# Kernel tuning notes

Hardware: AMD Instinct MI355X
Metric: run time of the kernel (lower is better)

Reference implementation:

```python
import jax, jax.numpy as jnp
import numpy as np

R, S, M, K = 512, 48, 4096, 16
RADIUS = 4.0 * 0.025
DIMS = [511, 256, 256, 256, 3]


def posenc(x, n_freqs):
    freqs = 2.0 ** jnp.arange(n_freqs, dtype=x.dtype)
    xf = x[..., None, :] * freqs[:, None]            # [..., F, C]
    sc = jnp.stack([jnp.sin(xf), jnp.cos(xf)], -2)   # [..., F, 2, C]
    return jnp.concatenate([x, sc.reshape(x.shape[:-1] + (-1,))], -1)


def ball_query(q, p, radius, k):
    # pytorch3d-style: first k points (by index order) within radius.
    # dists are squared distances, 0 for padding; neighbors are 0 for padding; idx -1 for padding.
    d2 = jnp.sum((q[:, None, :] - p[None, :, :]) ** 2, -1)    # [Nq, M]
    m = p.shape[0]
    order = jnp.where(d2 < radius * radius, jnp.arange(m), m)
    neg, idx = jax.lax.top_k(-order, k)                        # k smallest valid indices
    valid = neg > -m
    dists = jnp.where(valid, jnp.take_along_axis(d2, idx, axis=1), 0.0)
    nbrs = jnp.where(valid[..., None], p[idx], 0.0)
    return dists, jnp.where(valid, idx, -1), nbrs


def setup_inputs() -> dict:
    key = jax.random.key(0)
    ks = jax.random.split(key, 16)
    inp = {
        "points": jax.random.uniform(ks[0], (R, S, 3), jnp.float32),
        "normals": jax.random.normal(ks[1], (R * S, 3), jnp.float32),
        "view_dirs": jax.random.normal(ks[2], (R * S, 3), jnp.float32),
        "feature_vectors": jax.random.normal(ks[3], (R * S, 256), jnp.float32),
        "indices": 0,
        "physical_particles": jax.random.uniform(ks[4], (M, 3), jnp.float32),
        "rays": jax.random.normal(ks[5], (R, 6), jnp.float32),
        "ro": jax.random.normal(ks[6], (1, 3), jnp.float32),
    }
    for l in range(4):
        scale = (2.0 / DIMS[l + 1]) ** 0.5
        inp[f"W{l}"] = jax.random.normal(ks[7 + l], (DIMS[l + 1], DIMS[l]), jnp.float32) * scale
        inp[f"b{l}"] = jnp.zeros((DIMS[l + 1],), jnp.float32)
    return inp


def reference(points, normals, view_dirs, feature_vectors, indices, physical_particles,
              rays, ro, W0, b0, W1, b1, W2, b2, W3, b3):
    q = points.reshape(-1, 3)                                     # [R*S, 3]
    dists, idx, nbrs = ball_query(q, physical_particles, RADIUS, K)
    dists = dists.reshape(R, S, K)
    nbrs = nbrs.reshape(R, S, K, 3)
    nn_mask = dists != 0                                          # padded entries have dist 0
    num_nn = nn_mask.sum(-1, keepdims=True)                       # [R, S, 1]

    hit_pos_emb = posenc(q, 10)                                   # [R*S, 63]
    hit_dir_emb = jnp.repeat(posenc(rays[:, 3:], 4), S, axis=0)   # [R*S, 27]

    # smoothing_position (exclude_ray=True)
    dn = jnp.linalg.norm(nbrs - points[:, :, None, :], axis=-1)   # [R, S, K]
    w = jnp.maximum(1.0 - (dn / RADIUS) ** 3, 0.0)
    density = w.sum(-1, keepdims=True)                            # [R, S, 1]
    smoothed = (w[..., None] * nbrs).sum(-2) / (density + 1e-12)  # [R, S, 3]

    sp = smoothed.reshape(-1, 3)
    dirs = sp - ro
    dirs = dirs / jnp.linalg.norm(dirs, axis=-1, keepdims=True)

    density_emb = posenc(density.reshape(-1, 1), 4)               # [R*S, 9]
    smoothed_pos_emb = posenc(sp, 10)                             # [R*S, 63]

    # masked variance of neighbor offsets
    diff = jnp.where(nn_mask[..., None], nbrs - points[:, :, None, :], 0.0)
    mean = diff.sum(-2) / (num_nn + 1e-12)
    var = jnp.where(nn_mask[..., None], (diff - mean[:, :, None, :]) ** 2, 0.0).sum(-2) / (num_nn + 1e-12)
    var_emb = posenc(var.reshape(-1, 3), 10)                      # [R*S, 63]

    x = jnp.concatenate([hit_pos_emb, density_emb, smoothed_pos_emb, var_emb,
                         hit_dir_emb, posenc(dirs, 4), normals, feature_vectors], -1)  # [R*S, 511]

    for Wl, bl in ((W0, b0), (W1, b1), (W2, b2)):
        x = jax.nn.relu(x @ Wl.T + bl)
    return jax.nn.sigmoid(x @ W3.T + b3)
```

## Files before the change

kernel.cpp:

```cpp
#include <hip/hip_runtime.h>

typedef _Float16 f16;
typedef f16 f16x8 __attribute__((ext_vector_type(8)));
typedef float f32x4 __attribute__((ext_vector_type(4)));
typedef unsigned short u16;


struct FT {
  u16 v[256];
  static constexpr u16 enc(int s, int f, int k) {
    return (u16)(s | (f << 5) | (k << 9));
  }
  constexpr void p3(int base, int F, int src) {
    v[base + 0] = enc(src + 0, 0, 0);
    v[base + 1] = enc(src + 1, 0, 0);
    v[base + 2] = enc(src + 2, 0, 0);
    for (int f = 0; f < F; ++f)
      for (int r = 0; r < 6; ++r) {
        int comp = (r < 3) ? r : r - 3;
        v[base + 3 + f * 6 + r] = enc(src + comp, f, (r < 3) ? 1 : 2);
      }
  }
  constexpr void p1(int base, int F, int src) {
    v[base] = enc(src, 0, 0);
    for (int f = 0; f < F; ++f) {
      v[base + 1 + 2 * f] = enc(src, f, 1);
      v[base + 2 + 2 * f] = enc(src, f, 2);
    }
  }
  constexpr FT() : v{} {
    p3(0, 10, 0);
    p1(63, 4, 3);
    p3(72, 10, 4);
    p3(135, 10, 7);
    p3(198, 4, 10);
    p3(225, 4, 13);
    v[252] = enc(16, 0, 0);
    v[253] = enc(17, 0, 0);
    v[254] = enc(18, 0, 0);
    v[255] = enc(0, 0, 3);
  }
};
__constant__ FT ftab = FT();

__device__ float4 g_sorted[4096];
__device__ int    g_cellStart[1001];

__global__ __launch_bounds__(1024) void setup_kernel(
    const float* __restrict__ parts,
    const float* __restrict__ W0, const float* __restrict__ W1,
    const float* __restrict__ W2,
    f16* __restrict__ w0f, f16* __restrict__ w1f, f16* __restrict__ w2f)
{
  const int tid = threadIdx.x;
  if (blockIdx.x < 256) {
    int i = blockIdx.x * 1024 + tid;
    float v; f16* pf; int n, c;
    if (i < 131072) {
      n = i >> 9; c = i & 511;
      v = (c < 255) ? W0[n * 511 + c] : ((c == 255) ? 0.0f : W0[n * 511 + (c - 1)]);
      pf = w0f;
    } else if (i < 196608) {
      int j = i - 131072; n = j >> 8; c = j & 255; v = W1[j]; pf = w1f;
    } else {
      int j = i - 196608; n = j >> 8; c = j & 255; v = W2[j]; pf = w2f;
    }
    int kt = c >> 5, g = (c >> 3) & 3, jj = c & 7;
    int u = n * 4 + (g ^ ((n >> 1) & 3));
    pf[kt * 8192 + u * 8 + jj] = (f16)v;
  } else {
    __shared__ int cnt[1000];
    __shared__ int pos[1000];
    __shared__ int wpre[125];
    for (int j = tid; j < 1000; j += 1024) cnt[j] = 0;
    __syncthreads();

    float px[4], py[4], pz[4];
    int cd[4];
    #pragma unroll
    for (int t = 0; t < 4; ++t) {
      int i = tid + t * 1024;
      float x = parts[3 * i], y = parts[3 * i + 1], z = parts[3 * i + 2];
      int cx = min(max((int)(x * 10.0f), 0), 9);
      int cy = min(max((int)(y * 10.0f), 0), 9);
      int cz = min(max((int)(z * 10.0f), 0), 9);
      cd[t] = (cz * 10 + cy) * 10 + cx;
      px[t] = x; py[t] = y; pz[t] = z;
      atomicAdd(&cnt[cd[t]], 1);
    }
    __syncthreads();

    if (tid < 125) {
      int s = 0;
      #pragma unroll
      for (int k = 0; k < 8; ++k) s += cnt[tid * 8 + k];
      wpre[tid] = s;
    }
    __syncthreads();
    if (tid == 0) {
      int s = 0;
      for (int c = 0; c < 125; ++c) { int t = wpre[c]; wpre[c] = s; s += t; }
    }
    __syncthreads();
    if (tid < 125) {
      int run = wpre[tid];
      #pragma unroll
      for (int k = 0; k < 8; ++k) {
        int c = tid * 8 + k;
        int n = cnt[c];
        pos[c] = run;
        g_cellStart[c] = run;
        run += n;
      }
    }
    if (tid == 0) g_cellStart[1000] = 4096;
    __syncthreads();

    #pragma unroll
    for (int t = 0; t < 4; ++t) {
      int p = atomicAdd(&pos[cd[t]], 1);
      g_sorted[p] = make_float4(px[t], py[t], pz[t], __int_as_float(tid + t * 1024));
    }
  }
}

#define MAXCH 5

__global__ __launch_bounds__(512, 4) void fused_all(
    const float* __restrict__ points, const float* __restrict__ normals,
    const float* __restrict__ fvec, const float* __restrict__ rays,
    const float* __restrict__ ro, const float* __restrict__ parts,
    const f16* __restrict__ w0f, const f16* __restrict__ w1f,
    const f16* __restrict__ w2f,
    const float* __restrict__ b0, const float* __restrict__ b1,
    const float* __restrict__ b2,
    const float* __restrict__ W3, const float* __restrict__ b3,
    float* __restrict__ out)
{
  extern __shared__ char lds[];
  f16* As = (f16*)lds;
  f16* Hf = (f16*)lds;
  f16* H2 = (f16*)(lds + 24576);
  float* sdata = (float*)(lds + 49152);
  float* w3s = (float*)(lds + 49152);

  const int tid = threadIdx.x, lane = tid & 63, wn = tid >> 6;
  const int l15 = lane & 15, l4 = lane >> 4;
  const int blk = blockIdx.x;

  if (tid < 384) {
    int m = tid >> 3, sub = tid & 7, g = sub & 3, kh = sub >> 2;
    int u = m * 4 + (g ^ ((m >> 1) & 3));
    #pragma unroll
    for (int t = 0; t < 4; ++t) {
      int kf = kh * 4 + t;
      const float* src = fvec + (size_t)(blk * 48 + m) * 256 + kf * 32 + g * 8;
      float4 v0 = ((const float4*)src)[0];
      float4 v1 = ((const float4*)src)[1];
      f16 hs[8] = {(f16)v0.x, (f16)v0.y, (f16)v0.z, (f16)v0.w,
                   (f16)v1.x, (f16)v1.y, (f16)v1.z, (f16)v1.w};
      *(uint4*)(As + (8 + kf) * 1536 + u * 8) = *(uint4*)hs;
    }
  }

  const float RQ = 0.1f * 0.1f;
  #pragma unroll 1
  for (int t = 0; t < 6; ++t) {
    const int m48 = wn * 6 + t;
    const int q = blk * 48 + m48;
    const float qx = points[3 * q], qy = points[3 * q + 1], qz = points[3 * q + 2];

    int nAcc = 0;
    float sdx = 0, sdy = 0, sdz = 0;
    float s2x = 0, s2y = 0, s2z = 0;
    float sw = 0, swx = 0, swy = 0, swz = 0;

    const int cqx = min(max((int)(qx * 10.0f), 0), 9);
    const int cqy = min(max((int)(qy * 10.0f), 0), 9);
    const int cqz = min(max((int)(qz * 10.0f), 0), 9);

    int st_l = 0, cn_l = 0;
    if (lane < 9) {
      int dz = lane / 3, dy = lane - dz * 3;
      int cz = cqz - 1 + dz, cy = cqy - 1 + dy;
      if ((unsigned)cz <= 9u && (unsigned)cy <= 9u) {
        int x0 = max(cqx - 1, 0), x1 = min(cqx + 1, 9);
        int rb = (cz * 10 + cy) * 10;
        st_l = g_cellStart[rb + x0];
        cn_l = g_cellStart[rb + x1 + 1] - st_l;
      }
    }

    int pk[9], bk[9];
    int run = 0;
    #pragma unroll
    for (int k = 0; k < 9; ++k) {
      int stk = __builtin_amdgcn_readlane(st_l, k);
      int cnk = __builtin_amdgcn_readlane(cn_l, k);
      pk[k] = run;
      bk[k] = stk - run;
      run += cnk;
    }
    const int C = run;
    const bool fb = (C > MAXCH * 64);

    if (!fb) {
      float4 sv[MAXCH];
      int iv[MAXCH];
      unsigned long long hm[MAXCH];
      #pragma unroll
      for (int ch = 0; ch < MAXCH; ++ch) {
        if (ch * 64 < C) {
          int s = ch * 64 + lane;
          int g = bk[0];
          #pragma unroll
          for (int k = 1; k < 9; ++k) g = (s >= pk[k]) ? bk[k] : g;
          float4 pt = g_sorted[min(g + s, 4095)];
          if (s >= C) {
            pt.x = 1e9f; pt.y = 1e9f; pt.z = 1e9f;
            pt.w = __int_as_float(0x7fffffff);
          }
          sv[ch] = pt;
          iv[ch] = __float_as_int(pt.w);
          float ex = pt.x - qx, ey = pt.y - qy, ez = pt.z - qz;
          float d2 = __fadd_rn(__fadd_rn(__fmul_rn(ex, ex), __fmul_rn(ey, ey)),
                               __fmul_rn(ez, ez));
          hm[ch] = __ballot(d2 < RQ);
        } else {
          hm[ch] = 0ULL;
        }
      }

      int N = 0;
      #pragma unroll
      for (int ch = 0; ch < MAXCH; ++ch) N += __popcll(hm[ch]);

      int thr = 0x7fffffff;
      if (N > 16) {
        int lo = 0, hi = 4095;
        while (lo < hi) {
          int mid = (lo + hi) >> 1;
          int c = 0;
          #pragma unroll
          for (int ch = 0; ch < MAXCH; ++ch)
            if (ch * 64 < C)
              c += __popcll(hm[ch] & __ballot(iv[ch] <= mid));
          if (c >= 16) hi = mid; else lo = mid + 1;
        }
        thr = lo;
      }

      #pragma unroll
      for (int ch = 0; ch < MAXCH; ++ch) {
        if (ch * 64 < C) {
          float4 pt = sv[ch];
          float ex = pt.x - qx, ey = pt.y - qy, ez = pt.z - qz;
          float d2 = __fadd_rn(__fadd_rn(__fmul_rn(ex, ex), __fmul_rn(ey, ey)),
                               __fmul_rn(ez, ez));
          if (d2 < RQ && iv[ch] <= thr) {
            nAcc++;
            sdx += ex; sdy += ey; sdz += ez;
            s2x += ex * ex; s2y += ey * ey; s2z += ez * ez;
            float dn = sqrtf(d2);
            float tt = dn * 10.0f;
            float w = fmaxf(1.0f - tt * tt * tt, 0.0f);
            sw += w; swx += w * pt.x; swy += w * pt.y; swz += w * pt.z;
          }
        }
      }
    } else {
      int total = 0;
      for (int jr = 0; jr < 64; ++jr) {
        int pi = jr * 64 + lane;
        float x = parts[3 * pi], y = parts[3 * pi + 1], z = parts[3 * pi + 2];
        float ex = x - qx, ey = y - qy, ez = z - qz;
        float d2 = __fadd_rn(__fadd_rn(__fmul_rn(ex, ex), __fmul_rn(ey, ey)),
                             __fmul_rn(ez, ez));
        bool hit = d2 < RQ;
        unsigned long long m = __ballot(hit);
        int pos = __builtin_amdgcn_mbcnt_hi((unsigned)(m >> 32),
                  __builtin_amdgcn_mbcnt_lo((unsigned)m, 0u));
        if (hit && (total + pos < 16)) {
          nAcc++;
          sdx += ex; sdy += ey; sdz += ez;
          s2x += ex * ex; s2y += ey * ey; s2z += ez * ez;
          float dn = sqrtf(d2);
          float tt = dn * 10.0f;
          float w = fmaxf(1.0f - tt * tt * tt, 0.0f);
          sw += w; swx += w * x; swy += w * y; swz += w * z;
        }
        total += __popcll(m);
        if (total >= 16) break;
      }
    }

    #define WRED(x) { _Pragma("unroll") for (int o = 32; o; o >>= 1) x += __shfl_xor(x, o, 64); }
    float fn = (float)nAcc;
    WRED(fn); WRED(sdx); WRED(sdy); WRED(sdz);
    WRED(s2x); WRED(s2y); WRED(s2z);
    WRED(sw); WRED(swx); WRED(swy); WRED(swz);
    #undef WRED

    float tq = sqrtf(qx * qx + qy * qy + qz * qz) * 10.0f;
    float wpad = fmaxf(1.0f - tq * tq * tq, 0.0f);
    float density = sw + (16.0f - fn) * wpad;
    float invd = 1.0f / (density + 1e-12f);
    float spx = swx * invd, spy = swy * invd, spz = swz * invd;

    float invn = 1.0f / (fn + 1e-12f);
    float mx = sdx * invn, my = sdy * invn, mz = sdz * invn;
    float vx = fmaxf((s2x - 2.0f * mx * sdx + fn * mx * mx) * invn, 0.0f);
    float vy = fmaxf((s2y - 2.0f * my * sdy + fn * my * my) * invn, 0.0f);
    float vz = fmaxf((s2z - 2.0f * mz * sdz + fn * mz * mz) * invn, 0.0f);

    float dxx = spx - ro[0], dyy = spy - ro[1], dzz = spz - ro[2];
    float il = 1.0f / sqrtf(dxx * dxx + dyy * dyy + dzz * dzz);

    if (lane == 0) {
      float* s = sdata + m48 * 20;
      s[0] = qx; s[1] = qy; s[2] = qz; s[3] = density;
      s[4] = spx; s[5] = spy; s[6] = spz;
      s[7] = vx; s[8] = vy; s[9] = vz;
      s[10] = rays[6 * blk + 3]; s[11] = rays[6 * blk + 4]; s[12] = rays[6 * blk + 5];
      s[13] = dxx * il; s[14] = dyy * il; s[15] = dzz * il;
      s[16] = normals[3 * q]; s[17] = normals[3 * q + 1]; s[18] = normals[3 * q + 2];
    }
  }
  __syncthreads();

  #pragma unroll 1
  for (int t = 0; t < 6; ++t) {
    const int m48 = wn * 6 + t;
    const float* s = sdata + m48 * 20;
    #pragma unroll
    for (int it = 0; it < 4; ++it) {
      int c = it * 64 + lane;
      int e = ftab.v[c];
      float sv_ = s[e & 31];
      float arg = sv_ * (float)(1 << ((e >> 5) & 15));
      float sn, cs;
      __sincosf(arg, &sn, &cs);
      int kind = e >> 9;
      float val = (kind == 0) ? sv_ : (kind == 1 ? sn : (kind == 2 ? cs : 0.0f));
      int kt = c >> 5, g = (c >> 3) & 3, j = c & 7;
      int u = m48 * 4 + (g ^ ((m48 >> 1) & 3));
      As[kt * 1536 + u * 8 + j] = (f16)val;
    }
  }

  f32x4 acc[3][2];
  f16x8 bq[3][2];
  f16x8 af[2][3];

  int uB[2];
  #pragma unroll
  for (int j = 0; j < 2; ++j) {
    int n = wn * 32 + j * 16 + l15;
    uB[j] = n * 4 + (l4 ^ ((n >> 1) & 3));
  }
  int uA[3];
  #pragma unroll
  for (int i = 0; i < 3; ++i) {
    int m = i * 16 + l15;
    uA[i] = m * 4 + (l4 ^ ((m >> 1) & 3));
  }

  auto zacc = [&]() {
    #pragma unroll
    for (int i = 0; i < 3; ++i)
      #pragma unroll
      for (int j = 0; j < 2; ++j) acc[i][j] = (f32x4){0, 0, 0, 0};
  };
  auto loadB = [&](const f16* wf, int kt, f16x8* bf) {
    #pragma unroll
    for (int j = 0; j < 2; ++j)
      bf[j] = *(const f16x8*)(wf + kt * 8192 + uB[j] * 8);
  };
  auto loadA0 = [&](int kt, f16x8* a3) {
    #pragma unroll
    for (int i = 0; i < 3; ++i)
      a3[i] = *(const f16x8*)(As + kt * 1536 + uA[i] * 8);
  };
  auto loadAH = [&](const f16* Hsrc, int kt, f16x8* a3) {
    #pragma unroll
    for (int i = 0; i < 3; ++i) {
      int m = i * 16 + l15;
      int g = kt * 4 + l4;
      int u = m * 32 + (g ^ ((m >> 1) & 7));
      a3[i] = *(const f16x8*)(Hsrc + u * 8);
    }
  };
  auto mfmas = [&](f16x8* a3, f16x8* b2) {
    #pragma unroll
    for (int i = 0; i < 3; ++i)
      #pragma unroll
      for (int j = 0; j < 2; ++j)
        acc[i][j] = __builtin_amdgcn_mfma_f32_16x16x32_f16(a3[i], b2[j], acc[i][j], 0, 0, 0);
  };
  auto epilogue = [&](const float* bias_, f16* Hdst) {
    float bv[2];
    #pragma unroll
    for (int j = 0; j < 2; ++j) bv[j] = bias_[wn * 32 + j * 16 + l15];
    #pragma unroll
    for (int i = 0; i < 3; ++i) {
      #pragma unroll
      for (int r = 0; r < 4; ++r) {
        int m = i * 16 + l4 * 4 + r;
        #pragma unroll
        for (int j = 0; j < 2; ++j) {
          int n = wn * 32 + j * 16 + l15;
          float v = fmaxf(acc[i][j][r] + bv[j], 0.0f);
          int u = m * 32 + ((n >> 3) ^ ((m >> 1) & 7));
          Hdst[u * 8 + (n & 7)] = (f16)v;
        }
      }
    }
  };

  loadB(w0f, 0, bq[0]);
  loadB(w0f, 1, bq[1]);
  __syncthreads();

  zacc();
  loadA0(0, af[0]);
  #pragma unroll
  for (int kt = 0; kt < 16; ++kt) {
    if (kt < 14) loadB(w0f, kt + 2, bq[(kt + 2) % 3]);
    if (kt < 15) loadA0(kt + 1, af[(kt + 1) & 1]);
    mfmas(af[kt & 1], bq[kt % 3]);
  }
  loadB(w1f, 0, bq[0]);
  loadB(w1f, 1, bq[1]);
  __syncthreads();
  epilogue(b0, Hf);
  __syncthreads();

  zacc();
  loadAH(Hf, 0, af[0]);
  #pragma unroll
  for (int kt = 0; kt < 8; ++kt) {
    if (kt < 6) loadB(w1f, kt + 2, bq[(kt + 2) % 3]);
    if (kt < 7) loadAH(Hf, kt + 1, af[(kt + 1) & 1]);
    mfmas(af[kt & 1], bq[kt % 3]);
  }
  loadB(w2f, 0, bq[0]);
  loadB(w2f, 1, bq[1]);
  epilogue(b1, H2);
  __syncthreads();

  zacc();
  loadAH(H2, 0, af[0]);
  #pragma unroll
  for (int kt = 0; kt < 8; ++kt) {
    if (kt < 6) loadB(w2f, kt + 2, bq[(kt + 2) % 3]);
    if (kt < 7) loadAH(H2, kt + 1, af[(kt + 1) & 1]);
    mfmas(af[kt & 1], bq[kt % 3]);
  }
  epilogue(b2, Hf);
  __syncthreads();

  for (int i = tid; i < 768; i += 512) w3s[i] = W3[i];
  __syncthreads();

  const float B30 = b3[0], B31 = b3[1], B32 = b3[2];
  #pragma unroll 1
  for (int rr = 0; rr < 6; ++rr) {
    int m = wn * 6 + rr;
    int g = lane >> 1, j0 = (lane & 1) * 4;
    int u = m * 32 + (g ^ ((m >> 1) & 7));
    uint2 pk = *(const uint2*)(Hf + u * 8 + j0);
    f16 h4[4];
    *(uint2*)h4 = pk;
    float h0 = (float)h4[0], h1 = (float)h4[1], h2 = (float)h4[2], h3 = (float)h4[3];
    int kc = lane * 4;
    float4 wa = *(const float4*)(w3s + kc);
    float4 wb = *(const float4*)(w3s + 256 + kc);
    float4 wc = *(const float4*)(w3s + 512 + kc);
    float p0 = fmaf(h3, wa.w, fmaf(h2, wa.z, fmaf(h1, wa.y, h0 * wa.x)));
    float p1 = fmaf(h3, wb.w, fmaf(h2, wb.z, fmaf(h1, wb.y, h0 * wb.x)));
    float p2 = fmaf(h3, wc.w, fmaf(h2, wc.z, fmaf(h1, wc.y, h0 * wc.x)));
    #pragma unroll
    for (int o = 32; o; o >>= 1) {
      p0 += __shfl_xor(p0, o, 64);
      p1 += __shfl_xor(p1, o, 64);
      p2 += __shfl_xor(p2, o, 64);
    }
    if (lane == 0) {
      size_t ro_ = (size_t)(blk * 48 + m) * 3;
      out[ro_ + 0] = 1.0f / (1.0f + expf(-(p0 + B30)));
      out[ro_ + 1] = 1.0f / (1.0f + expf(-(p1 + B31)));
      out[ro_ + 2] = 1.0f / (1.0f + expf(-(p2 + B32)));
    }
  }
}

extern "C" void kernel_launch(void* const* d_in, const int* in_sizes, int n_in,
                              void* d_out, int out_size, void* d_ws, size_t ws_size,
                              hipStream_t stream) {
  const float* points  = (const float*)d_in[0];
  const float* normals = (const float*)d_in[1];
  const float* fvec    = (const float*)d_in[3];
  const float* parts   = (const float*)d_in[5];
  const float* rays    = (const float*)d_in[6];
  const float* ro      = (const float*)d_in[7];
  const float* W0 = (const float*)d_in[8];
  const float* b0 = (const float*)d_in[9];
  const float* W1 = (const float*)d_in[10];
  const float* b1 = (const float*)d_in[11];
  const float* W2 = (const float*)d_in[12];
  const float* b2 = (const float*)d_in[13];
  const float* W3 = (const float*)d_in[14];
  const float* b3 = (const float*)d_in[15];

  char* ws = (char*)d_ws;
  f16* w0f = (f16*)(ws);
  f16* w1f = (f16*)(ws + 262144);
  f16* w2f = (f16*)(ws + 393216);
  float* out = (float*)d_out;

  (void)hipFuncSetAttribute((const void*)fused_all,
                            hipFuncAttributeMaxDynamicSharedMemorySize, 52992);

  setup_kernel<<<257, 1024, 0, stream>>>(parts, W0, W1, W2, w0f, w1f, w2f);
  fused_all<<<512, 512, 52992, stream>>>(points, normals, fvec, rays, ro, parts,
                                         w0f, w1f, w2f,
                                         b0, b1, b2, W3, b3, out);
}
```

Before: 151.0 us.

## Use MFMA for final layer, parallel prefix scan, iterative top-k pruning

The final 256->3 layer now runs as an f16 MFMA on three waves, using a W3 copy pre-packed by an extra setup block, instead of per-row fp32 dot products with wave reductions. The serial single-thread prefix sum in the grid-binning setup becomes a parallel Hillis-Steele scan. The binary search for the 16th-smallest neighbor index becomes repeated removal of the current maximum index until 16 hits remain. The last change does more work when many neighbors are in range, and the final layer now runs in f16 with the accuracy loss that brings.

```diff
diff --git a/kernel.cpp b/kernel.cpp
--- a/kernel.cpp
+++ b/kernel.cpp
@@ -49,8 +49,9 @@
 __global__ __launch_bounds__(1024) void setup_kernel(
     const float* __restrict__ parts,
     const float* __restrict__ W0, const float* __restrict__ W1,
-    const float* __restrict__ W2,
-    f16* __restrict__ w0f, f16* __restrict__ w1f, f16* __restrict__ w2f)
+    const float* __restrict__ W2, const float* __restrict__ W3,
+    f16* __restrict__ w0f, f16* __restrict__ w1f, f16* __restrict__ w2f,
+    f16* __restrict__ w3f)
 {
   const int tid = threadIdx.x;
   if (blockIdx.x < 256) {
@@ -68,7 +69,7 @@
     int kt = c >> 5, g = (c >> 3) & 3, jj = c & 7;
     int u = n * 4 + (g ^ ((n >> 1) & 3));
     pf[kt * 8192 + u * 8 + jj] = (f16)v;
-  } else {
+  } else if (blockIdx.x == 256) {
     __shared__ int cnt[1000];
     __shared__ int pos[1000];
     __shared__ int wpre[125];
@@ -90,20 +91,23 @@
     }
     __syncthreads();
 
+    int own = 0;
     if (tid < 125) {
-      int s = 0;
-      #pragma unroll
-      for (int k = 0; k < 8; ++k) s += cnt[tid * 8 + k];
-      wpre[tid] = s;
+      #pragma unroll
+      for (int k = 0; k < 8; ++k) own += cnt[tid * 8 + k];
+      wpre[tid] = own;
     }
     __syncthreads();
-    if (tid == 0) {
-      int s = 0;
-      for (int c = 0; c < 125; ++c) { int t = wpre[c]; wpre[c] = s; s += t; }
-    }
-    __syncthreads();
+    #pragma unroll
+    for (int off = 1; off < 128; off <<= 1) {
+      int v = 0;
+      if (tid < 125 && tid >= off) v = wpre[tid - off];
+      __syncthreads();
+      if (tid < 125) wpre[tid] += v;
+      __syncthreads();
+    }
     if (tid < 125) {
-      int run = wpre[tid];
+      int run = wpre[tid] - own;
       #pragma unroll
       for (int k = 0; k < 8; ++k) {
         int c = tid * 8 + k;
@@ -121,6 +125,16 @@
       int p = atomicAdd(&pos[cd[t]], 1);
       g_sorted[p] = make_float4(px[t], py[t], pz[t], __int_as_float(tid + t * 1024));
     }
+  } else {
+    #pragma unroll
+    for (int t = 0; t < 4; ++t) {
+      int e = tid * 4 + t;
+      int n = e >> 8, c = e & 255;
+      float v = (n < 3) ? W3[n * 256 + c] : 0.0f;
+      int kt = c >> 5, g = (c >> 3) & 3, jj = c & 7;
+      int u = n * 4 + (g ^ ((n >> 1) & 3));
+      w3f[kt * 512 + u * 8 + jj] = (f16)v;
+    }
   }
 }
 
@@ -131,10 +145,9 @@
     const float* __restrict__ fvec, const float* __restrict__ rays,
     const float* __restrict__ ro, const float* __restrict__ parts,
     const f16* __restrict__ w0f, const f16* __restrict__ w1f,
-    const f16* __restrict__ w2f,
+    const f16* __restrict__ w2f, const f16* __restrict__ w3f,
     const float* __restrict__ b0, const float* __restrict__ b1,
-    const float* __restrict__ b2,
-    const float* __restrict__ W3, const float* __restrict__ b3,
+    const float* __restrict__ b2, const float* __restrict__ b3,
     float* __restrict__ out)
 {
   extern __shared__ char lds[];
@@ -142,7 +155,6 @@
   f16* Hf = (f16*)lds;
   f16* H2 = (f16*)(lds + 24576);
   float* sdata = (float*)(lds + 49152);
-  float* w3s = (float*)(lds + 49152);
 
   const int tid = threadIdx.x, lane = tid & 63, wn = tid >> 6;
   const int l15 = lane & 15, l4 = lane >> 4;
@@ -208,6 +220,7 @@
       float4 sv[MAXCH];
       int iv[MAXCH];
       unsigned long long hm[MAXCH];
+      unsigned hb = 0;
       #pragma unroll
       for (int ch = 0; ch < MAXCH; ++ch) {
         if (ch * 64 < C) {
@@ -225,9 +238,12 @@
           float ex = pt.x - qx, ey = pt.y - qy, ez = pt.z - qz;
           float d2 = __fadd_rn(__fadd_rn(__fmul_rn(ex, ex), __fmul_rn(ey, ey)),
                                __fmul_rn(ez, ez));
-          hm[ch] = __ballot(d2 < RQ);
+          bool hit = d2 < RQ;
+          if (hit) hb |= (1u << ch);
+          hm[ch] = __ballot(hit);
         } else {
           hm[ch] = 0ULL;
+          iv[ch] = 0x7fffffff;
         }
       }
 
@@ -235,19 +251,17 @@
       #pragma unroll
       for (int ch = 0; ch < MAXCH; ++ch) N += __popcll(hm[ch]);
 
-      int thr = 0x7fffffff;
-      if (N > 16) {
-        int lo = 0, hi = 4095;
-        while (lo < hi) {
-          int mid = (lo + hi) >> 1;
-          int c = 0;
-          #pragma unroll
-          for (int ch = 0; ch < MAXCH; ++ch)
-            if (ch * 64 < C)
-              c += __popcll(hm[ch] & __ballot(iv[ch] <= mid));
-          if (c >= 16) hi = mid; else lo = mid + 1;
-        }
-        thr = lo;
+      while (N > 16) {
+        int mi = -1;
+        #pragma unroll
+        for (int ch = 0; ch < MAXCH; ++ch)
+          if ((hb >> ch) & 1) mi = max(mi, iv[ch]);
+        #pragma unroll
+        for (int o = 32; o; o >>= 1) mi = max(mi, __shfl_xor(mi, o, 64));
+        #pragma unroll
+        for (int ch = 0; ch < MAXCH; ++ch)
+          if (((hb >> ch) & 1) && iv[ch] == mi) hb &= ~(1u << ch);
+        --N;
       }
 
       #pragma unroll
@@ -257,7 +271,7 @@
           float ex = pt.x - qx, ey = pt.y - qy, ez = pt.z - qz;
           float d2 = __fadd_rn(__fadd_rn(__fmul_rn(ex, ex), __fmul_rn(ey, ey)),
                                __fmul_rn(ez, ez));
-          if (d2 < RQ && iv[ch] <= thr) {
+          if ((hb >> ch) & 1) {
             nAcc++;
             sdx += ex; sdy += ey; sdz += ez;
             s2x += ex * ex; s2y += ey * ey; s2z += ez * ez;
@@ -459,37 +473,26 @@
   epilogue(b2, Hf);
   __syncthreads();
 
-  for (int i = tid; i < 768; i += 512) w3s[i] = W3[i];
-  __syncthreads();
-
-  const float B30 = b3[0], B31 = b3[1], B32 = b3[2];
-  #pragma unroll 1
-  for (int rr = 0; rr < 6; ++rr) {
-    int m = wn * 6 + rr;
-    int g = lane >> 1, j0 = (lane & 1) * 4;
-    int u = m * 32 + (g ^ ((m >> 1) & 7));
-    uint2 pk = *(const uint2*)(Hf + u * 8 + j0);
-    f16 h4[4];
-    *(uint2*)h4 = pk;
-    float h0 = (float)h4[0], h1 = (float)h4[1], h2 = (float)h4[2], h3 = (float)h4[3];
-    int kc = lane * 4;
-    float4 wa = *(const float4*)(w3s + kc);
-    float4 wb = *(const float4*)(w3s + 256 + kc);
-    float4 wc = *(const float4*)(w3s + 512 + kc);
-    float p0 = fmaf(h3, wa.w, fmaf(h2, wa.z, fmaf(h1, wa.y, h0 * wa.x)));
-    float p1 = fmaf(h3, wb.w, fmaf(h2, wb.z, fmaf(h1, wb.y, h0 * wb.x)));
-    float p2 = fmaf(h3, wc.w, fmaf(h2, wc.z, fmaf(h1, wc.y, h0 * wc.x)));
-    #pragma unroll
-    for (int o = 32; o; o >>= 1) {
-      p0 += __shfl_xor(p0, o, 64);
-      p1 += __shfl_xor(p1, o, 64);
-      p2 += __shfl_xor(p2, o, 64);
-    }
-    if (lane == 0) {
-      size_t ro_ = (size_t)(blk * 48 + m) * 3;
-      out[ro_ + 0] = 1.0f / (1.0f + expf(-(p0 + B30)));
-      out[ro_ + 1] = 1.0f / (1.0f + expf(-(p1 + B31)));
-      out[ro_ + 2] = 1.0f / (1.0f + expf(-(p2 + B32)));
+  if (wn < 3) {
+    f32x4 a3c = (f32x4){0, 0, 0, 0};
+    int uB3 = l15 * 4 + (l4 ^ ((l15 >> 1) & 3));
+    #pragma unroll
+    for (int kt = 0; kt < 8; ++kt) {
+      int m = wn * 16 + l15;
+      int g = kt * 4 + l4;
+      int u = m * 32 + (g ^ ((m >> 1) & 7));
+      f16x8 a = *(const f16x8*)(Hf + u * 8);
+      f16x8 b = *(const f16x8*)(w3f + kt * 512 + uB3 * 8);
+      a3c = __builtin_amdgcn_mfma_f32_16x16x32_f16(a, b, a3c, 0, 0, 0);
+    }
+    if (l15 < 3) {
+      float bias = b3[l15];
+      #pragma unroll
+      for (int r = 0; r < 4; ++r) {
+        int m = wn * 16 + l4 * 4 + r;
+        out[(size_t)(blk * 48 + m) * 3 + l15] =
+            1.0f / (1.0f + expf(-(a3c[r] + bias)));
+      }
     }
   }
 }
@@ -516,13 +519,15 @@
   f16* w0f = (f16*)(ws);
   f16* w1f = (f16*)(ws + 262144);
   f16* w2f = (f16*)(ws + 393216);
+  f16* w3f = (f16*)(ws + 524288);
   float* out = (float*)d_out;
 
   (void)hipFuncSetAttribute((const void*)fused_all,
                             hipFuncAttributeMaxDynamicSharedMemorySize, 52992);
 
-  setup_kernel<<<257, 1024, 0, stream>>>(parts, W0, W1, W2, w0f, w1f, w2f);
+  setup_kernel<<<258, 1024, 0, stream>>>(parts, W0, W1, W2, W3,
+                                         w0f, w1f, w2f, w3f);
   fused_all<<<512, 512, 52992, stream>>>(points, normals, fvec, rays, ro, parts,
-                                         w0f, w1f, w2f,
-                                         b0, b1, b2, W3, b3, out);
+                                         w0f, w1f, w2f, w3f,
+                                         b0, b1, b2, b3, out);
 }
```

Measured after the change: 152.3 us. Within noise of the previous version (+0.9%).
